# Kernel tuning notes

Measured on AMD Instinct MI355X. Metric: run time of the kernel, lower is better.

Reference implementation:

```python
import jax, jax.numpy as jnp
import numpy as np


def setup_inputs() -> dict:
    key = jax.random.key(0)
    ks = jax.random.split(key, 6)
    N, E, F, H, HOP = 100000, 1600000, 128, 128, 3
    x = jax.random.normal(ks[0], (N, F), dtype=jnp.float32)
    edge_index = jax.random.randint(ks[1], (2, E), 0, N, dtype=jnp.int64)
    # per-hop weights, scaled like nn.Linear default init magnitude
    W1 = jax.random.normal(ks[2], (HOP, H, F), dtype=jnp.float32) * (1.0 / np.sqrt(F))
    W2 = jax.random.normal(ks[3], (HOP, H, H), dtype=jnp.float32) * (1.0 / np.sqrt(H))
    W3 = jax.random.normal(ks[4], (HOP, H, H), dtype=jnp.float32) * (1.0 / np.sqrt(H))
    W4 = jax.random.normal(ks[5], (HOP, H, 1), dtype=jnp.float32)
    return {"x": x, "edge_index": edge_index, "W1": W1, "W2": W2, "W3": W3, "W4": W4}


def reference(x, edge_index, W1, W2, W3, W4):
    N = x.shape[0]
    E = edge_index.shape[1]
    H = W1.shape[1]
    hop = W1.shape[0]
    row, col = edge_index[0], edge_index[1]
    edge_attr = jnp.ones((E, 1), dtype=x.dtype)  # as in original forward
    h = jnp.zeros((N, H), dtype=x.dtype)  # initial node_embedding
    for i in range(hop):
        node_feat = x @ W1[i].T                                   # [N,H]
        # gather neighbor embeddings then scatter-sum to destination nodes
        nbr_agg = jax.ops.segment_sum(h[col], row, num_segments=N)  # [N,H]
        edge_emb = jax.nn.relu(edge_attr @ W4[i].T)               # [E,H]
        edge_agg = jax.ops.segment_sum(edge_emb, row, num_segments=N)  # [N,H]
        h = jax.nn.relu(node_feat + nbr_agg @ W2[i].T + edge_agg @ W3[i].T)
        # dropout is identity in eval mode
    return h
```

## Files before the change

kernel.cpp:

```cpp
#include <hip/hip_runtime.h>

#define H 128

typedef __attribute__((ext_vector_type(8))) short bf16x8;
typedef __attribute__((ext_vector_type(4))) float f32x4;
typedef unsigned int uint;
typedef unsigned short ushort;

__device__ __forceinline__ ushort f2bf(float f) {
    uint u = __builtin_bit_cast(uint, f);
    uint r = u + 0x7FFFu + ((u >> 16) & 1u);
    return (ushort)(r >> 16);
}
__device__ __forceinline__ float bf_lo(uint u) {
    return __builtin_bit_cast(float, u << 16);
}
__device__ __forceinline__ float bf_hi(uint u) {
    return __builtin_bit_cast(float, u & 0xFFFF0000u);
}


__global__ void bucket_hist(const int* __restrict__ ei, int E, int NB, int NBLK,
                            int* __restrict__ cntg) {
    __shared__ int cnt[1024];
    int blk = blockIdx.x, t = threadIdx.x;
    for (int b = t; b < NB; b += 256) cnt[b] = 0;
    __syncthreads();
    int lo = blk << 13, hi = min(lo + 8192, E);
    for (int e = lo + t; e < hi; e += 256) atomicAdd(&cnt[ei[e] >> 10], 1);
    __syncthreads();
    for (int b = t; b < NB; b += 256) cntg[b * NBLK + blk] = cnt[b];
}

__global__ void scan_reduce(const int* __restrict__ src, int* __restrict__ bsum, int M) {
    __shared__ int sm[256];
    int lo = blockIdx.x * 512;
    int t = threadIdx.x;
    int a = (lo + t < M) ? src[lo + t] : 0;
    int b = (lo + 256 + t < M) ? src[lo + 256 + t] : 0;
    sm[t] = a + b;
    __syncthreads();
    for (int d = 128; d; d >>= 1) {
        if (t < d) sm[t] += sm[t + d];
        __syncthreads();
    }
    if (t == 0) bsum[blockIdx.x] = sm[0];
}

__global__ void scan_bsums(int* __restrict__ bsum, int* __restrict__ dst, int B, int M) {
    __shared__ int s[1024];
    int t = threadIdx.x;
    int v = (t < B) ? bsum[t] : 0;
    s[t] = v;
    __syncthreads();
    for (int d = 1; d < 1024; d <<= 1) {
        int u = (t >= d) ? s[t - d] : 0;
        __syncthreads();
        s[t] += u;
        __syncthreads();
    }
    if (t < B) bsum[t] = s[t] - v;
    if (t == 1023) dst[M] = s[1023];
}

__global__ void scan_write(const int* __restrict__ src, const int* __restrict__ bsum,
                           int* __restrict__ dst, int M) {
    __shared__ int sm[256];
    int lo = blockIdx.x * 512;
    int t = threadIdx.x;
    int i0 = lo + 2 * t, i1 = i0 + 1;
    int d0 = (i0 < M) ? src[i0] : 0;
    int d1 = (i1 < M) ? src[i1] : 0;
    int p = d0 + d1;
    sm[t] = p;
    __syncthreads();
    for (int d = 1; d < 256; d <<= 1) {
        int u = (t >= d) ? sm[t - d] : 0;
        __syncthreads();
        sm[t] += u;
        __syncthreads();
    }
    int ex = sm[t] - p + bsum[blockIdx.x];
    if (i0 < M) dst[i0] = ex;
    if (i1 < M) dst[i1] = ex + d0;
}

__global__ void bucket_scatter(const int* __restrict__ ei, int E, int NB, int NBLK,
                               const int* __restrict__ ebase, int2* __restrict__ ebuf) {
    __shared__ int lcnt[1024];
    __shared__ int lbase[1024];
    int blk = blockIdx.x, t = threadIdx.x;
    for (int b = t; b < NB; b += 256) {
        lcnt[b] = 0;
        lbase[b] = ebase[b * NBLK + blk];
    }
    __syncthreads();
    int lo = blk << 13, hi = min(lo + 8192, E);
    for (int e = lo + t; e < hi; e += 256) {
        int r = ei[e], c = ei[E + e];
        int b = r >> 10;
        int pos = lbase[b] + atomicAdd(&lcnt[b], 1);
        ebuf[pos] = make_int2(r, c);
    }
}

__global__ void bucket_csr(const int2* __restrict__ ebuf, const int* __restrict__ ebase,
                           int NB, int NBLK, int E, int N,
                           int* __restrict__ deg, int* __restrict__ off,
                           int* __restrict__ colss) {
    __shared__ int rcnt[1024], rloff[1024], tsum[256];
    int b = blockIdx.x, t = threadIdx.x;
    int rowbase = b << 10;
    int rs = ebase[b * NBLK];
    int re = (b == NB - 1) ? E : ebase[(b + 1) * NBLK];
    for (int i = t; i < 1024; i += 256) rcnt[i] = 0;
    __syncthreads();
    for (int e = rs + t; e < re; e += 256) atomicAdd(&rcnt[ebuf[e].x - rowbase], 1);
    __syncthreads();
    int s = 0, part[4];
#pragma unroll
    for (int k = 0; k < 4; ++k) { part[k] = s; s += rcnt[t * 4 + k]; }
    tsum[t] = s;
    __syncthreads();
    int self = s;
    for (int d = 1; d < 256; d <<= 1) {
        int v = (t >= d) ? tsum[t - d] : 0;
        __syncthreads();
        tsum[t] += v;
        __syncthreads();
    }
    int pre = tsum[t] - self;
#pragma unroll
    for (int k = 0; k < 4; ++k) {
        int lr = t * 4 + k, row = rowbase + lr;
        rloff[lr] = pre + part[k];
        if (row < N) {
            deg[row] = rcnt[lr];
            off[row] = rs + rloff[lr];
        }
    }
    if (b == NB - 1 && t == 0) off[N] = E;
    __syncthreads();
    for (int i = t; i < 1024; i += 256) rcnt[i] = 0;
    __syncthreads();
    for (int e = rs + t; e < re; e += 256) {
        int2 rc = ebuf[e];
        int lr = rc.x - rowbase;
        int pz = atomicAdd(&rcnt[lr], 1);
        colss[rs + rloff[lr] + pz] = rc.y;
    }
}

__global__ void cvec_kernel(const float* __restrict__ W3, const float* __restrict__ W4,
                            float* __restrict__ cvec) {
    int i = blockIdx.x, k = threadIdx.x;
    const float* w3 = W3 + i * H * H + k * H;
    const float* w4 = W4 + i * H;
    float s = 0.f;
    for (int j = 0; j < H; ++j) s += w3[j] * fmaxf(w4[j], 0.f);
    cvec[i * H + k] = s;
}

__global__ void cast_bf16(const float* __restrict__ in, ushort* __restrict__ outp, int n8) {
    int i = blockIdx.x * blockDim.x + threadIdx.x;
    if (i >= n8) return;
    const float4* in4 = (const float4*)in;
    float4 a = in4[2 * i], b = in4[2 * i + 1];
    uint4 o;
    o.x = (uint)f2bf(a.x) | ((uint)f2bf(a.y) << 16);
    o.y = (uint)f2bf(a.z) | ((uint)f2bf(a.w) << 16);
    o.z = (uint)f2bf(b.x) | ((uint)f2bf(b.y) << 16);
    o.w = (uint)f2bf(b.z) | ((uint)f2bf(b.w) << 16);
    ((uint4*)outp)[i] = o;
}


template<int ADD_DEGC, int RELU, int OUT_BF16>
__global__ __launch_bounds__(256)
void gemm_mfma(const ushort* __restrict__ A, const ushort* __restrict__ W,
               const int* __restrict__ deg, const float* __restrict__ cvec,
               void* __restrict__ Cout, int N)
{
    __shared__ uint4 A4[128 * 8];
    __shared__ uint4 W4[128 * 8];
    int t = threadIdx.x;
    int w = t >> 6, l = t & 63;
    int lg = l >> 4, lr = l & 15;
    int rowBase = blockIdx.x * 128;

    f32x4 acc[2][8];
#pragma unroll
    for (int rt = 0; rt < 2; ++rt)
#pragma unroll
        for (int ct = 0; ct < 8; ++ct) acc[rt][ct] = (f32x4){0.f, 0.f, 0.f, 0.f};

    const uint4* Ag = (const uint4*)A;
    const uint4* Wg = (const uint4*)W;

    for (int kc = 0; kc < 2; ++kc) {
        if (kc) __syncthreads();
#pragma unroll
        for (int it = 0; it < 4; ++it) {
            int idx = it * 256 + t;
            int r = idx >> 3, s = idx & 7;
            int gr = rowBase + r;
            uint4 v = make_uint4(0, 0, 0, 0);
            if (gr < N) v = Ag[(size_t)gr * 16 + kc * 8 + s];
            A4[r * 8 + (s ^ (r & 7))] = v;
            W4[r * 8 + (s ^ (r & 7))] = Wg[r * 16 + kc * 8 + s];
        }
        __syncthreads();
#pragma unroll
        for (int kk = 0; kk < 2; ++kk) {
            int slot = kk * 4 + lg;
            bf16x8 af[2], bfr[8];
#pragma unroll
            for (int rt = 0; rt < 2; ++rt) {
                int r = w * 32 + rt * 16 + lr;
                af[rt] = *(const bf16x8*)&A4[r * 8 + (slot ^ (r & 7))];
            }
#pragma unroll
            for (int ct = 0; ct < 8; ++ct) {
                int r = ct * 16 + lr;
                bfr[ct] = *(const bf16x8*)&W4[r * 8 + (slot ^ (r & 7))];
            }
#pragma unroll
            for (int rt = 0; rt < 2; ++rt)
#pragma unroll
                for (int ct = 0; ct < 8; ++ct)
                    acc[rt][ct] = __builtin_amdgcn_mfma_f32_16x16x32_bf16(
                        af[rt], bfr[ct], acc[rt][ct], 0, 0, 0);
        }
    }

    float cv[8];
    if (ADD_DEGC) {
#pragma unroll
        for (int ct = 0; ct < 8; ++ct) cv[ct] = cvec[ct * 16 + lr];
    }
#pragma unroll
    for (int rt = 0; rt < 2; ++rt) {
#pragma unroll
        for (int j = 0; j < 4; ++j) {
            int gr = rowBase + w * 32 + rt * 16 + lg * 4 + j;
            if (gr < N) {
                float d = ADD_DEGC ? (float)deg[gr] : 0.f;
#pragma unroll
                for (int ct = 0; ct < 8; ++ct) {
                    int gc = ct * 16 + lr;
                    float v = acc[rt][ct][j];
                    if (ADD_DEGC) v += d * cv[ct];
                    if (RELU) v = fmaxf(v, 0.f);
                    if (OUT_BF16) ((ushort*)Cout)[(size_t)gr * H + gc] = f2bf(v);
                    else ((float*)Cout)[(size_t)gr * H + gc] = v;
                }
            }
        }
    }
}


template<int OUT_BF16>
__global__ void aggregate_relu3(const ushort* __restrict__ biasb, const ushort* __restrict__ p,
                                const int* __restrict__ off, const int* __restrict__ cols,
                                void* __restrict__ dst, int N)
{
    int node = blockIdx.x * 4 + (threadIdx.x >> 6);
    if (node >= N) return;
    int l = threadIdx.x & 63;
    int s = off[node], e = off[node + 1];
    const uint* pu = (const uint*)p;
    float ax = 0.f, ay = 0.f;
    int i = s;
    for (; i + 8 <= e; i += 8) {
        uint v0 = pu[(size_t)cols[i]     * 64 + l];
        uint v1 = pu[(size_t)cols[i + 1] * 64 + l];
        uint v2 = pu[(size_t)cols[i + 2] * 64 + l];
        uint v3 = pu[(size_t)cols[i + 3] * 64 + l];
        uint v4 = pu[(size_t)cols[i + 4] * 64 + l];
        uint v5 = pu[(size_t)cols[i + 5] * 64 + l];
        uint v6 = pu[(size_t)cols[i + 6] * 64 + l];
        uint v7 = pu[(size_t)cols[i + 7] * 64 + l];
        ax += bf_lo(v0) + bf_lo(v1) + bf_lo(v2) + bf_lo(v3)
            + bf_lo(v4) + bf_lo(v5) + bf_lo(v6) + bf_lo(v7);
        ay += bf_hi(v0) + bf_hi(v1) + bf_hi(v2) + bf_hi(v3)
            + bf_hi(v4) + bf_hi(v5) + bf_hi(v6) + bf_hi(v7);
    }
    for (; i + 4 <= e; i += 4) {
        uint v0 = pu[(size_t)cols[i]     * 64 + l];
        uint v1 = pu[(size_t)cols[i + 1] * 64 + l];
        uint v2 = pu[(size_t)cols[i + 2] * 64 + l];
        uint v3 = pu[(size_t)cols[i + 3] * 64 + l];
        ax += bf_lo(v0) + bf_lo(v1) + bf_lo(v2) + bf_lo(v3);
        ay += bf_hi(v0) + bf_hi(v1) + bf_hi(v2) + bf_hi(v3);
    }
    for (; i < e; ++i) {
        uint v = pu[(size_t)cols[i] * 64 + l];
        ax += bf_lo(v);
        ay += bf_hi(v);
    }
    uint bb = ((const uint*)biasb)[(size_t)node * 64 + l];
    float ox = fmaxf(bf_lo(bb) + ax, 0.f);
    float oy = fmaxf(bf_hi(bb) + ay, 0.f);
    if (OUT_BF16) {
        ((uint*)dst)[(size_t)node * 64 + l] = (uint)f2bf(ox) | ((uint)f2bf(oy) << 16);
    } else {
        ((float2*)dst)[(size_t)node * 64 + l] = make_float2(ox, oy);
    }
}


extern "C" void kernel_launch(void* const* d_in, const int* in_sizes, int n_in,
                              void* d_out, int out_size, void* d_ws, size_t ws_size,
                              hipStream_t stream)
{
    const float* x  = (const float*)d_in[0];
    const int*   ei = (const int*)d_in[1];
    const float* W1 = (const float*)d_in[2];
    const float* W2 = (const float*)d_in[3];
    const float* W3 = (const float*)d_in[4];
    const float* W4 = (const float*)d_in[5];
    int N   = in_sizes[0] / H;
    int E   = in_sizes[1] / 2;
    int HOP = in_sizes[2] / (H * H);

    int NB   = (N + 1023) >> 10;
    int NBLK = (E + 8191) >> 13;
    int M    = NB * NBLK;

    char* ws = (char*)d_ws;
    int*   deg   = (int*)ws;
    int*   off   = deg + N;
    int*   colss = off + N + 1;
    int*   cntg  = colss + E;
    int*   ebase = cntg + M;
    int*   bsum  = ebase + M + 1;
    float* cvec  = (float*)(bsum + 1024);
    size_t fo = (((size_t)((char*)(cvec + HOP * H) - ws)) + 255) & ~(size_t)255;
    int2*  ebuf  = (int2*)(ws + fo);
    ushort* xb   = (ushort*)(ebuf + E);
    ushort* W1b  = xb + (size_t)N * H;
    ushort* W2b  = W1b + (size_t)HOP * H * H;
    ushort* p    = W2b + (size_t)HOP * H * H;
    ushort* h    = p + (size_t)N * H;
    ushort* bias = h + (size_t)N * H;

    bucket_hist<<<NBLK, 256, 0, stream>>>(ei, E, NB, NBLK, cntg);
    int Bq = (M + 511) / 512;
    scan_reduce<<<Bq, 256, 0, stream>>>(cntg, bsum, M);
    scan_bsums<<<1, 1024, 0, stream>>>(bsum, ebase, Bq, M);
    scan_write<<<Bq, 256, 0, stream>>>(cntg, bsum, ebase, M);
    bucket_scatter<<<NBLK, 256, 0, stream>>>(ei, E, NB, NBLK, ebase, ebuf);
    bucket_csr<<<NB, 256, 0, stream>>>(ebuf, ebase, NB, NBLK, E, N, deg, off, colss);

    cvec_kernel<<<HOP, H, 0, stream>>>(W3, W4, cvec);

    int nx8 = N * H / 8;
    cast_bf16<<<(nx8 + 255) / 256, 256, 0, stream>>>(x, xb, nx8);
    int nw8 = HOP * H * H / 8;
    cast_bf16<<<(nw8 + 255) / 256, 256, 0, stream>>>(W1, W1b, nw8);
    cast_bf16<<<(nw8 + 255) / 256, 256, 0, stream>>>(W2, W2b, nw8);

    int gblocks = (N + 127) / 128;
    float* out = (float*)d_out;

    if (HOP == 1) {
        gemm_mfma<1, 1, 0><<<gblocks, 256, 0, stream>>>(xb, W1b, deg, cvec, out, N);
        return;
    }
    gemm_mfma<1, 1, 1><<<gblocks, 256, 0, stream>>>(xb, W1b, deg, cvec, h, N);

    for (int i = 1; i < HOP; ++i) {
        int last = (i == HOP - 1);
        gemm_mfma<0, 0, 1><<<gblocks, 256, 0, stream>>>(h, W2b + (size_t)i * H * H,
                                                        nullptr, nullptr, p, N);
        gemm_mfma<1, 0, 1><<<gblocks, 256, 0, stream>>>(xb, W1b + (size_t)i * H * H,
                                                        deg, cvec + i * H, bias, N);
        if (last)
            aggregate_relu3<0><<<(N + 3) / 4, 256, 0, stream>>>(bias, p, off, colss, out, N);
        else
            aggregate_relu3<1><<<(N + 3) / 4, 256, 0, stream>>>(bias, p, off, colss, h, N);
    }
}
```

Baseline: 305.1 us.

## Fuse x cast with all per-hop x projections in one kernel, retune CSR build

Adds a multi_xproj kernel that loads each x tile once, casts it to bf16 in shared memory, and computes the x@W1 projections for every hop, writing h for hop 0 and a per-hop bias buffer for the later hops. This removes the separate x cast pass and the repeated bf16 x reads in each hop's GEMM. The edge bucketing chunk is halved to give more blocks, and bucket_csr now uses 1024 threads with a single flat scan. The bias buffer now holds (HOP-1) slices of N*H, so the workspace must be large enough for it.

New measurement: 270.5 us. -11.4%, faster.

```diff
diff --git a/kernel.cpp b/kernel.cpp
--- a/kernel.cpp
+++ b/kernel.cpp
@@ -26,7 +26,7 @@
     int blk = blockIdx.x, t = threadIdx.x;
     for (int b = t; b < NB; b += 256) cnt[b] = 0;
     __syncthreads();
-    int lo = blk << 13, hi = min(lo + 8192, E);
+    int lo = blk << 12, hi = min(lo + 4096, E);
     for (int e = lo + t; e < hi; e += 256) atomicAdd(&cnt[ei[e] >> 10], 1);
     __syncthreads();
     for (int b = t; b < NB; b += 256) cntg[b * NBLK + blk] = cnt[b];
@@ -95,7 +95,7 @@
         lbase[b] = ebase[b * NBLK + blk];
     }
     __syncthreads();
-    int lo = blk << 13, hi = min(lo + 8192, E);
+    int lo = blk << 12, hi = min(lo + 4096, E);
     for (int e = lo + t; e < hi; e += 256) {
         int r = ei[e], c = ei[E + e];
         int b = r >> 10;
@@ -104,46 +104,41 @@
     }
 }
 
-__global__ void bucket_csr(const int2* __restrict__ ebuf, const int* __restrict__ ebase,
-                           int NB, int NBLK, int E, int N,
-                           int* __restrict__ deg, int* __restrict__ off,
-                           int* __restrict__ colss) {
-    __shared__ int rcnt[1024], rloff[1024], tsum[256];
+__global__ __launch_bounds__(1024)
+void bucket_csr(const int2* __restrict__ ebuf, const int* __restrict__ ebase,
+                int NB, int NBLK, int E, int N,
+                int* __restrict__ deg, int* __restrict__ off,
+                int* __restrict__ colss) {
+    __shared__ int rcnt[1024], rloff[1024];
     int b = blockIdx.x, t = threadIdx.x;
     int rowbase = b << 10;
     int rs = ebase[b * NBLK];
     int re = (b == NB - 1) ? E : ebase[(b + 1) * NBLK];
-    for (int i = t; i < 1024; i += 256) rcnt[i] = 0;
-    __syncthreads();
-    for (int e = rs + t; e < re; e += 256) atomicAdd(&rcnt[ebuf[e].x - rowbase], 1);
-    __syncthreads();
-    int s = 0, part[4];
-#pragma unroll
-    for (int k = 0; k < 4; ++k) { part[k] = s; s += rcnt[t * 4 + k]; }
-    tsum[t] = s;
-    __syncthreads();
-    int self = s;
-    for (int d = 1; d < 256; d <<= 1) {
-        int v = (t >= d) ? tsum[t - d] : 0;
-        __syncthreads();
-        tsum[t] += v;
-        __syncthreads();
-    }
-    int pre = tsum[t] - self;
-#pragma unroll
-    for (int k = 0; k < 4; ++k) {
-        int lr = t * 4 + k, row = rowbase + lr;
-        rloff[lr] = pre + part[k];
-        if (row < N) {
-            deg[row] = rcnt[lr];
-            off[row] = rs + rloff[lr];
-        }
+    rcnt[t] = 0;
+    __syncthreads();
+    for (int e = rs + t; e < re; e += 1024) atomicAdd(&rcnt[ebuf[e].x - rowbase], 1);
+    __syncthreads();
+    int v = rcnt[t];
+    rloff[t] = v;
+    __syncthreads();
+    for (int d = 1; d < 1024; d <<= 1) {
+        int u = (t >= d) ? rloff[t - d] : 0;
+        __syncthreads();
+        rloff[t] += u;
+        __syncthreads();
+    }
+    int ex = rloff[t] - v;
+    int row = rowbase + t;
+    if (row < N) {
+        deg[row] = v;
+        off[row] = rs + ex;
     }
     if (b == NB - 1 && t == 0) off[N] = E;
     __syncthreads();
-    for (int i = t; i < 1024; i += 256) rcnt[i] = 0;
-    __syncthreads();
-    for (int e = rs + t; e < re; e += 256) {
+    rloff[t] = ex;
+    rcnt[t] = 0;
+    __syncthreads();
+    for (int e = rs + t; e < re; e += 1024) {
         int2 rc = ebuf[e];
         int lr = rc.x - rowbase;
         int pz = atomicAdd(&rcnt[lr], 1);
@@ -172,6 +167,124 @@
     o.z = (uint)f2bf(b.x) | ((uint)f2bf(b.y) << 16);
     o.w = (uint)f2bf(b.z) | ((uint)f2bf(b.w) << 16);
     ((uint4*)outp)[i] = o;
+}
+
+
+__global__ __launch_bounds__(256)
+void multi_xproj(const float* __restrict__ x, const ushort* __restrict__ W1b,
+                 const int* __restrict__ deg, const float* __restrict__ cvec,
+                 ushort* __restrict__ h, ushort* __restrict__ bias,
+                 float* __restrict__ outf, int N, int HOP)
+{
+    __shared__ uint4 A4[128 * 16];
+    __shared__ uint4 W4s[128 * 16];
+    int t = threadIdx.x;
+    int wv = t >> 6, l = t & 63;
+    int lg = l >> 4, lr = l & 15;
+    int rowBase = blockIdx.x * 128;
+
+    const float4* xg = (const float4*)x;
+    const uint4* Wg = (const uint4*)W1b;
+
+#pragma unroll
+    for (int it = 0; it < 8; ++it) {
+        int idx = it * 256 + t;
+        int r = idx >> 4, s = idx & 15;
+        int gr = rowBase + r;
+        uint4 v = make_uint4(0, 0, 0, 0);
+        if (gr < N) {
+            float4 a = xg[(size_t)gr * 32 + 2 * s];
+            float4 b = xg[(size_t)gr * 32 + 2 * s + 1];
+            v.x = (uint)f2bf(a.x) | ((uint)f2bf(a.y) << 16);
+            v.y = (uint)f2bf(a.z) | ((uint)f2bf(a.w) << 16);
+            v.z = (uint)f2bf(b.x) | ((uint)f2bf(b.y) << 16);
+            v.w = (uint)f2bf(b.z) | ((uint)f2bf(b.w) << 16);
+        }
+        A4[r * 16 + (s ^ (r & 7))] = v;
+    }
+#pragma unroll
+    for (int it = 0; it < 8; ++it) {
+        int idx = it * 256 + t;
+        int r = idx >> 4, s = idx & 15;
+        W4s[r * 16 + (s ^ (r & 7))] = Wg[r * 16 + s];
+    }
+    __syncthreads();
+
+    float dreg[2][4];
+#pragma unroll
+    for (int rt = 0; rt < 2; ++rt)
+#pragma unroll
+        for (int jj = 0; jj < 4; ++jj) {
+            int gr = rowBase + wv * 32 + rt * 16 + lg * 4 + jj;
+            dreg[rt][jj] = (gr < N) ? (float)deg[gr] : 0.f;
+        }
+
+    for (int j = 0; j < HOP; ++j) {
+        f32x4 acc[2][8];
+#pragma unroll
+        for (int rt = 0; rt < 2; ++rt)
+#pragma unroll
+            for (int ct = 0; ct < 8; ++ct) acc[rt][ct] = (f32x4){0.f, 0.f, 0.f, 0.f};
+
+#pragma unroll
+        for (int ks = 0; ks < 4; ++ks) {
+            int slot = ks * 4 + lg;
+            bf16x8 af[2], bfr[8];
+#pragma unroll
+            for (int rt = 0; rt < 2; ++rt) {
+                int r = wv * 32 + rt * 16 + lr;
+                af[rt] = *(const bf16x8*)&A4[r * 16 + (slot ^ (r & 7))];
+            }
+#pragma unroll
+            for (int ct = 0; ct < 8; ++ct) {
+                int r = ct * 16 + lr;
+                bfr[ct] = *(const bf16x8*)&W4s[r * 16 + (slot ^ (r & 7))];
+            }
+#pragma unroll
+            for (int rt = 0; rt < 2; ++rt)
+#pragma unroll
+                for (int ct = 0; ct < 8; ++ct)
+                    acc[rt][ct] = __builtin_amdgcn_mfma_f32_16x16x32_bf16(
+                        af[rt], bfr[ct], acc[rt][ct], 0, 0, 0);
+        }
+
+        if (j + 1 < HOP) {
+            __syncthreads();
+#pragma unroll
+            for (int it = 0; it < 8; ++it) {
+                int idx = it * 256 + t;
+                int r = idx >> 4, s = idx & 15;
+                W4s[r * 16 + (s ^ (r & 7))] = Wg[((j + 1) * 128 + r) * 16 + s];
+            }
+        }
+
+        float cv[8];
+#pragma unroll
+        for (int ct = 0; ct < 8; ++ct) cv[ct] = cvec[j * H + ct * 16 + lr];
+#pragma unroll
+        for (int rt = 0; rt < 2; ++rt) {
+#pragma unroll
+            for (int jj = 0; jj < 4; ++jj) {
+                int gr = rowBase + wv * 32 + rt * 16 + lg * 4 + jj;
+                if (gr < N) {
+                    float d = dreg[rt][jj];
+#pragma unroll
+                    for (int ct = 0; ct < 8; ++ct) {
+                        int gc = ct * 16 + lr;
+                        float v = acc[rt][ct][jj] + d * cv[ct];
+                        if (j == 0) {
+                            v = fmaxf(v, 0.f);
+                            if (HOP == 1) outf[(size_t)gr * H + gc] = v;
+                            else h[(size_t)gr * H + gc] = f2bf(v);
+                        } else {
+                            bias[(size_t)(j - 1) * N * H + (size_t)gr * H + gc] = f2bf(v);
+                        }
+                    }
+                }
+            }
+        }
+        if (j + 1 < HOP) __syncthreads();
+    }
 }
 
 
@@ -325,7 +438,7 @@
     int HOP = in_sizes[2] / (H * H);
 
     int NB   = (N + 1023) >> 10;
-    int NBLK = (E + 8191) >> 13;
+    int NBLK = (E + 4095) >> 12;
     int M    = NB * NBLK;
 
     char* ws = (char*)d_ws;
@@ -338,8 +451,7 @@
     float* cvec  = (float*)(bsum + 1024);
     size_t fo = (((size_t)((char*)(cvec + HOP * H) - ws)) + 255) & ~(size_t)255;
     int2*  ebuf  = (int2*)(ws + fo);
-    ushort* xb   = (ushort*)(ebuf + E);
-    ushort* W1b  = xb + (size_t)N * H;
+    ushort* W1b  = (ushort*)(ebuf + E);
     ushort* W2b  = W1b + (size_t)HOP * H * H;
     ushort* p    = W2b + (size_t)HOP * H * H;
     ushort* h    = p + (size_t)N * H;
@@ -351,12 +463,10 @@
     scan_bsums<<<1, 1024, 0, stream>>>(bsum, ebase, Bq, M);
     scan_write<<<Bq, 256, 0, stream>>>(cntg, bsum, ebase, M);
     bucket_scatter<<<NBLK, 256, 0, stream>>>(ei, E, NB, NBLK, ebase, ebuf);
-    bucket_csr<<<NB, 256, 0, stream>>>(ebuf, ebase, NB, NBLK, E, N, deg, off, colss);
+    bucket_csr<<<NB, 1024, 0, stream>>>(ebuf, ebase, NB, NBLK, E, N, deg, off, colss);
 
     cvec_kernel<<<HOP, H, 0, stream>>>(W3, W4, cvec);
 
-    int nx8 = N * H / 8;
-    cast_bf16<<<(nx8 + 255) / 256, 256, 0, stream>>>(x, xb, nx8);
     int nw8 = HOP * H * H / 8;
     cast_bf16<<<(nw8 + 255) / 256, 256, 0, stream>>>(W1, W1b, nw8);
     cast_bf16<<<(nw8 + 255) / 256, 256, 0, stream>>>(W2, W2b, nw8);
@@ -364,21 +474,18 @@
     int gblocks = (N + 127) / 128;
     float* out = (float*)d_out;
 
-    if (HOP == 1) {
-        gemm_mfma<1, 1, 0><<<gblocks, 256, 0, stream>>>(xb, W1b, deg, cvec, out, N);
-        return;
-    }
-    gemm_mfma<1, 1, 1><<<gblocks, 256, 0, stream>>>(xb, W1b, deg, cvec, h, N);
+    multi_xproj<<<gblocks, 256, 0, stream>>>(x, W1b, deg, cvec, h, bias, out, N, HOP);
+    if (HOP == 1) return;
 
     for (int i = 1; i < HOP; ++i) {
         int last = (i == HOP - 1);
         gemm_mfma<0, 0, 1><<<gblocks, 256, 0, stream>>>(h, W2b + (size_t)i * H * H,
                                                         nullptr, nullptr, p, N);
-        gemm_mfma<1, 0, 1><<<gblocks, 256, 0, stream>>>(xb, W1b + (size_t)i * H * H,
-                                                        deg, cvec + i * H, bias, N);
         if (last)
-            aggregate_relu3<0><<<(N + 3) / 4, 256, 0, stream>>>(bias, p, off, colss, out, N);
+            aggregate_relu3<0><<<(N + 3) / 4, 256, 0, stream>>>(bias + (size_t)(i - 1) * N * H,
+                                                                p, off, colss, out, N);
         else
-            aggregate_relu3<1><<<(N + 3) / 4, 256, 0, stream>>>(bias, p, off, colss, h, N);
-    }
-}
+            aggregate_relu3<1><<<(N + 3) / 4, 256, 0, stream>>>(bias + (size_t)(i - 1) * N * H,
+                                                                p, off, colss, h, N);
+    }
+}
```

## Aggregate before projection and fuse both hop GEMMs into one K-concatenated kernel

Applied to the files above, without the earlier changes.

Each hop now first sums neighbour embeddings (aggregate-then-transform) and then runs a single GEMM that accumulates x·W1ᵀ and agg·W2ᵀ with the degree/cvec bias and ReLU in the epilogue. This replaces two separate GEMMs plus a bias buffer round trip with one GEMM, which saves a launch and a full N×H read and write. The aggregated sum is rounded to bf16 before the W2 product, which changes where rounding happens. The CSR build also switches to 1024-thread blocks with a single-level scan, and the edge chunk size is halved.

Result: faster. 260.7 us (-14.6%).

```diff
diff --git a/kernel.cpp b/kernel.cpp
--- a/kernel.cpp
+++ b/kernel.cpp
@@ -26,7 +26,7 @@
     int blk = blockIdx.x, t = threadIdx.x;
     for (int b = t; b < NB; b += 256) cnt[b] = 0;
     __syncthreads();
-    int lo = blk << 13, hi = min(lo + 8192, E);
+    int lo = blk << 12, hi = min(lo + 4096, E);
     for (int e = lo + t; e < hi; e += 256) atomicAdd(&cnt[ei[e] >> 10], 1);
     __syncthreads();
     for (int b = t; b < NB; b += 256) cntg[b * NBLK + blk] = cnt[b];
@@ -95,7 +95,7 @@
         lbase[b] = ebase[b * NBLK + blk];
     }
     __syncthreads();
-    int lo = blk << 13, hi = min(lo + 8192, E);
+    int lo = blk << 12, hi = min(lo + 4096, E);
     for (int e = lo + t; e < hi; e += 256) {
         int r = ei[e], c = ei[E + e];
         int b = r >> 10;
@@ -104,46 +104,41 @@
     }
 }
 
-__global__ void bucket_csr(const int2* __restrict__ ebuf, const int* __restrict__ ebase,
-                           int NB, int NBLK, int E, int N,
-                           int* __restrict__ deg, int* __restrict__ off,
-                           int* __restrict__ colss) {
-    __shared__ int rcnt[1024], rloff[1024], tsum[256];
+__global__ __launch_bounds__(1024)
+void bucket_csr(const int2* __restrict__ ebuf, const int* __restrict__ ebase,
+                int NB, int NBLK, int E, int N,
+                int* __restrict__ deg, int* __restrict__ off,
+                int* __restrict__ colss) {
+    __shared__ int rcnt[1024], rloff[1024];
     int b = blockIdx.x, t = threadIdx.x;
     int rowbase = b << 10;
     int rs = ebase[b * NBLK];
     int re = (b == NB - 1) ? E : ebase[(b + 1) * NBLK];
-    for (int i = t; i < 1024; i += 256) rcnt[i] = 0;
-    __syncthreads();
-    for (int e = rs + t; e < re; e += 256) atomicAdd(&rcnt[ebuf[e].x - rowbase], 1);
-    __syncthreads();
-    int s = 0, part[4];
-#pragma unroll
-    for (int k = 0; k < 4; ++k) { part[k] = s; s += rcnt[t * 4 + k]; }
-    tsum[t] = s;
-    __syncthreads();
-    int self = s;
-    for (int d = 1; d < 256; d <<= 1) {
-        int v = (t >= d) ? tsum[t - d] : 0;
-        __syncthreads();
-        tsum[t] += v;
-        __syncthreads();
-    }
-    int pre = tsum[t] - self;
-#pragma unroll
-    for (int k = 0; k < 4; ++k) {
-        int lr = t * 4 + k, row = rowbase + lr;
-        rloff[lr] = pre + part[k];
-        if (row < N) {
-            deg[row] = rcnt[lr];
-            off[row] = rs + rloff[lr];
-        }
+    rcnt[t] = 0;
+    __syncthreads();
+    for (int e = rs + t; e < re; e += 1024) atomicAdd(&rcnt[ebuf[e].x - rowbase], 1);
+    __syncthreads();
+    int v = rcnt[t];
+    rloff[t] = v;
+    __syncthreads();
+    for (int d = 1; d < 1024; d <<= 1) {
+        int u = (t >= d) ? rloff[t - d] : 0;
+        __syncthreads();
+        rloff[t] += u;
+        __syncthreads();
+    }
+    int ex = rloff[t] - v;
+    int row = rowbase + t;
+    if (row < N) {
+        deg[row] = v;
+        off[row] = rs + ex;
     }
     if (b == NB - 1 && t == 0) off[N] = E;
     __syncthreads();
-    for (int i = t; i < 1024; i += 256) rcnt[i] = 0;
-    __syncthreads();
-    for (int e = rs + t; e < re; e += 256) {
+    rloff[t] = ex;
+    rcnt[t] = 0;
+    __syncthreads();
+    for (int e = rs + t; e < re; e += 1024) {
         int2 rc = ebuf[e];
         int lr = rc.x - rowbase;
         int pz = atomicAdd(&rcnt[lr], 1);
@@ -175,14 +170,15 @@
 }
 
 
-template<int ADD_DEGC, int RELU, int OUT_BF16>
+template<int RELU, int OUT_BF16>
 __global__ __launch_bounds__(256)
-void gemm_mfma(const ushort* __restrict__ A, const ushort* __restrict__ W,
-               const int* __restrict__ deg, const float* __restrict__ cvec,
-               void* __restrict__ Cout, int N)
+void gemm_pairs(const ushort* __restrict__ A0, const ushort* __restrict__ W0,
+                const ushort* __restrict__ A1, const ushort* __restrict__ W1,
+                int npairs, const int* __restrict__ deg, const float* __restrict__ cvec,
+                void* __restrict__ Cout, int N)
 {
-    __shared__ uint4 A4[128 * 8];
-    __shared__ uint4 W4[128 * 8];
+    __shared__ uint4 A4[1024];
+    __shared__ uint4 W4[1024];
     int t = threadIdx.x;
     int w = t >> 6, l = t & 63;
     int lg = l >> 4, lr = l & 15;
@@ -194,62 +190,60 @@
 #pragma unroll
         for (int ct = 0; ct < 8; ++ct) acc[rt][ct] = (f32x4){0.f, 0.f, 0.f, 0.f};
 
-    const uint4* Ag = (const uint4*)A;
-    const uint4* Wg = (const uint4*)W;
-
-    for (int kc = 0; kc < 2; ++kc) {
-        if (kc) __syncthreads();
-#pragma unroll
-        for (int it = 0; it < 4; ++it) {
-            int idx = it * 256 + t;
-            int r = idx >> 3, s = idx & 7;
-            int gr = rowBase + r;
-            uint4 v = make_uint4(0, 0, 0, 0);
-            if (gr < N) v = Ag[(size_t)gr * 16 + kc * 8 + s];
-            A4[r * 8 + (s ^ (r & 7))] = v;
-            W4[r * 8 + (s ^ (r & 7))] = Wg[r * 16 + kc * 8 + s];
+    for (int pr = 0; pr < npairs; ++pr) {
+        const uint4* Ag = (const uint4*)(pr ? A1 : A0);
+        const uint4* Wg = (const uint4*)(pr ? W1 : W0);
+        for (int kc = 0; kc < 2; ++kc) {
+            if (pr || kc) __syncthreads();
+#pragma unroll
+            for (int it = 0; it < 4; ++it) {
+                int idx = it * 256 + t;
+                int r = idx >> 3, s = idx & 7;
+                int gr = rowBase + r;
+                uint4 v = make_uint4(0, 0, 0, 0);
+                if (gr < N) v = Ag[(size_t)gr * 16 + kc * 8 + s];
+                A4[r * 8 + (s ^ (r & 7))] = v;
+                W4[r * 8 + (s ^ (r & 7))] = Wg[r * 16 + kc * 8 + s];
+            }
+            __syncthreads();
+#pragma unroll
+            for (int kk = 0; kk < 2; ++kk) {
+                int slot = kk * 4 + lg;
+                bf16x8 af[2], bfr[8];
+#pragma unroll
+                for (int rt = 0; rt < 2; ++rt) {
+                    int r = w * 32 + rt * 16 + lr;
+                    af[rt] = *(const bf16x8*)&A4[r * 8 + (slot ^ (r & 7))];
+                }
+#pragma unroll
+                for (int ct = 0; ct < 8; ++ct) {
+                    int r = ct * 16 + lr;
+                    bfr[ct] = *(const bf16x8*)&W4[r * 8 + (slot ^ (r & 7))];
+                }
+#pragma unroll
+                for (int rt = 0; rt < 2; ++rt)
+#pragma unroll
+                    for (int ct = 0; ct < 8; ++ct)
+                        acc[rt][ct] = __builtin_amdgcn_mfma_f32_16x16x32_bf16(
+                            af[rt], bfr[ct], acc[rt][ct], 0, 0, 0);
+            }
         }
-        __syncthreads();
-#pragma unroll
-        for (int kk = 0; kk < 2; ++kk) {
-            int slot = kk * 4 + lg;
-            bf16x8 af[2], bfr[8];
-#pragma unroll
-            for (int rt = 0; rt < 2; ++rt) {
-                int r = w * 32 + rt * 16 + lr;
-                af[rt] = *(const bf16x8*)&A4[r * 8 + (slot ^ (r & 7))];
-            }
-#pragma unroll
-            for (int ct = 0; ct < 8; ++ct) {
-                int r = ct * 16 + lr;
-                bfr[ct] = *(const bf16x8*)&W4[r * 8 + (slot ^ (r & 7))];
-            }
-#pragma unroll
-            for (int rt = 0; rt < 2; ++rt)
-#pragma unroll
-                for (int ct = 0; ct < 8; ++ct)
-                    acc[rt][ct] = __builtin_amdgcn_mfma_f32_16x16x32_bf16(
-                        af[rt], bfr[ct], acc[rt][ct], 0, 0, 0);
-        }
     }
 
     float cv[8];
-    if (ADD_DEGC) {
-#pragma unroll
-        for (int ct = 0; ct < 8; ++ct) cv[ct] = cvec[ct * 16 + lr];
-    }
+#pragma unroll
+    for (int ct = 0; ct < 8; ++ct) cv[ct] = cvec[ct * 16 + lr];
 #pragma unroll
     for (int rt = 0; rt < 2; ++rt) {
 #pragma unroll
         for (int j = 0; j < 4; ++j) {
             int gr = rowBase + w * 32 + rt * 16 + lg * 4 + j;
             if (gr < N) {
-                float d = ADD_DEGC ? (float)deg[gr] : 0.f;
+                float d = (float)deg[gr];
 #pragma unroll
                 for (int ct = 0; ct < 8; ++ct) {
                     int gc = ct * 16 + lr;
-                    float v = acc[rt][ct][j];
-                    if (ADD_DEGC) v += d * cv[ct];
+                    float v = acc[rt][ct][j] + d * cv[ct];
                     if (RELU) v = fmaxf(v, 0.f);
                     if (OUT_BF16) ((ushort*)Cout)[(size_t)gr * H + gc] = f2bf(v);
                     else ((float*)Cout)[(size_t)gr * H + gc] = v;
@@ -260,16 +254,15 @@
 }
 
 
-template<int OUT_BF16>
-__global__ void aggregate_relu3(const ushort* __restrict__ biasb, const ushort* __restrict__ p,
-                                const int* __restrict__ off, const int* __restrict__ cols,
-                                void* __restrict__ dst, int N)
+__global__ void aggregate_sum(const ushort* __restrict__ hsrc,
+                              const int* __restrict__ off, const int* __restrict__ cols,
+                              ushort* __restrict__ sdst, int N)
 {
     int node = blockIdx.x * 4 + (threadIdx.x >> 6);
     if (node >= N) return;
     int l = threadIdx.x & 63;
     int s = off[node], e = off[node + 1];
-    const uint* pu = (const uint*)p;
+    const uint* pu = (const uint*)hsrc;
     float ax = 0.f, ay = 0.f;
     int i = s;
     for (; i + 8 <= e; i += 8) {
@@ -299,14 +292,7 @@
         ax += bf_lo(v);
         ay += bf_hi(v);
     }
-    uint bb = ((const uint*)biasb)[(size_t)node * 64 + l];
-    float ox = fmaxf(bf_lo(bb) + ax, 0.f);
-    float oy = fmaxf(bf_hi(bb) + ay, 0.f);
-    if (OUT_BF16) {
-        ((uint*)dst)[(size_t)node * 64 + l] = (uint)f2bf(ox) | ((uint)f2bf(oy) << 16);
-    } else {
-        ((float2*)dst)[(size_t)node * 64 + l] = make_float2(ox, oy);
-    }
+    ((uint*)sdst)[(size_t)node * 64 + l] = (uint)f2bf(ax) | ((uint)f2bf(ay) << 16);
 }
 
 
@@ -325,7 +311,7 @@
     int HOP = in_sizes[2] / (H * H);
 
     int NB   = (N + 1023) >> 10;
-    int NBLK = (E + 8191) >> 13;
+    int NBLK = (E + 4095) >> 12;
     int M    = NB * NBLK;
 
     char* ws = (char*)d_ws;
@@ -338,12 +324,11 @@
     float* cvec  = (float*)(bsum + 1024);
     size_t fo = (((size_t)((char*)(cvec + HOP * H) - ws)) + 255) & ~(size_t)255;
     int2*  ebuf  = (int2*)(ws + fo);
-    ushort* xb   = (ushort*)(ebuf + E);
-    ushort* W1b  = xb + (size_t)N * H;
+    ushort* W1b  = (ushort*)(ebuf + E);
     ushort* W2b  = W1b + (size_t)HOP * H * H;
-    ushort* p    = W2b + (size_t)HOP * H * H;
-    ushort* h    = p + (size_t)N * H;
-    ushort* bias = h + (size_t)N * H;
+    ushort* xb   = W2b + (size_t)HOP * H * H;
+    ushort* h    = xb + (size_t)N * H;
+    ushort* sagg = h + (size_t)N * H;
 
     bucket_hist<<<NBLK, 256, 0, stream>>>(ei, E, NB, NBLK, cntg);
     int Bq = (M + 511) / 512;
@@ -351,7 +336,7 @@
     scan_bsums<<<1, 1024, 0, stream>>>(bsum, ebase, Bq, M);
     scan_write<<<Bq, 256, 0, stream>>>(cntg, bsum, ebase, M);
     bucket_scatter<<<NBLK, 256, 0, stream>>>(ei, E, NB, NBLK, ebase, ebuf);
-    bucket_csr<<<NB, 256, 0, stream>>>(ebuf, ebase, NB, NBLK, E, N, deg, off, colss);
+    bucket_csr<<<NB, 1024, 0, stream>>>(ebuf, ebase, NB, NBLK, E, N, deg, off, colss);
 
     cvec_kernel<<<HOP, H, 0, stream>>>(W3, W4, cvec);
 
@@ -365,20 +350,23 @@
     float* out = (float*)d_out;
 
     if (HOP == 1) {
-        gemm_mfma<1, 1, 0><<<gblocks, 256, 0, stream>>>(xb, W1b, deg, cvec, out, N);
+        gemm_pairs<1, 0><<<gblocks, 256, 0, stream>>>(xb, W1b, nullptr, nullptr, 1,
+                                                      deg, cvec, out, N);
         return;
     }
-    gemm_mfma<1, 1, 1><<<gblocks, 256, 0, stream>>>(xb, W1b, deg, cvec, h, N);
+    gemm_pairs<1, 1><<<gblocks, 256, 0, stream>>>(xb, W1b, nullptr, nullptr, 1,
+                                                  deg, cvec, h, N);
 
     for (int i = 1; i < HOP; ++i) {
         int last = (i == HOP - 1);
-        gemm_mfma<0, 0, 1><<<gblocks, 256, 0, stream>>>(h, W2b + (size_t)i * H * H,
-                                                        nullptr, nullptr, p, N);
-        gemm_mfma<1, 0, 1><<<gblocks, 256, 0, stream>>>(xb, W1b + (size_t)i * H * H,
-                                                        deg, cvec + i * H, bias, N);
+        aggregate_sum<<<(N + 3) / 4, 256, 0, stream>>>(h, off, colss, sagg, N);
         if (last)
-            aggregate_relu3<0><<<(N + 3) / 4, 256, 0, stream>>>(bias, p, off, colss, out, N);
+            gemm_pairs<1, 0><<<gblocks, 256, 0, stream>>>(xb, W1b + (size_t)i * H * H,
+                                                          sagg, W2b + (size_t)i * H * H,
+                                                          2, deg, cvec + i * H, out, N);
         else
-            aggregate_relu3<1><<<(N + 3) / 4, 256, 0, stream>>>(bias, p, off, colss, h, N);
-    }
-}
+            gemm_pairs<1, 1><<<gblocks, 256, 0, stream>>>(xb, W1b + (size_t)i * H * H,
+                                                          sagg, W2b + (size_t)i * H * H,
+                                                          2, deg, cvec + i * H, h, N);
+    }
+}
```
